# Kernel tuning notes

Measured on AMD Instinct MI355X. Metric: run time of the kernel, lower is better.

The kernel has to match this reference:

```python
import jax, jax.numpy as jnp
import numpy as np

N, E = 16384, 524288
IN_C, H1, H2 = 128, 128, 64
EDGE_F = 16
NB = 10                      # binary outputs
MC_GROUPS = (4, 6)           # multi-class group sizes (proto, service)
NC = 10                      # continuous outputs
EPS = 1e-5


def setup_inputs() -> dict:
    key = jax.random.key(0)
    ks = jax.random.split(key, 16)
    def lin(k, fan_in, fan_out):
        s = 1.0 / np.sqrt(fan_in)
        kw, kb = jax.random.split(k)
        return (jax.random.uniform(kw, (fan_in, fan_out), jnp.float32, -s, s),
                jax.random.uniform(kb, (fan_out,), jnp.float32, -s, s))
    w1, b1 = lin(ks[0], IN_C, H1)
    w2, b2 = lin(ks[1], H1, H2)
    w_bin, b_bin = lin(ks[2], H2, NB)
    w_mc, b_mc = lin(ks[3], H2, sum(MC_GROUPS))
    w_cont, b_cont = lin(ks[4], H2, NC)
    w_edge, b_edge = lin(ks[5], 2 * H2, EDGE_F)
    return {
        "x": jax.random.normal(ks[6], (N, IN_C), jnp.float32),
        "edge_index": jax.random.randint(ks[7], (2, E), 0, N, jnp.int64),
        "edge_attr": jax.random.normal(ks[8], (E, EDGE_F), jnp.float32),
        "w1": w1, "b1": b1,
        "bn1_g": jnp.ones((H1,), jnp.float32), "bn1_b": jnp.zeros((H1,), jnp.float32),
        "w2": w2, "b2": b2,
        "bn2_g": jnp.ones((H2,), jnp.float32), "bn2_b": jnp.zeros((H2,), jnp.float32),
        "w_bin": w_bin, "b_bin": b_bin,
        "w_mc": w_mc, "b_mc": b_mc,
        "w_cont": w_cont, "b_cont": b_cont,
        "w_edge": w_edge, "b_edge": b_edge,
    }


def _gcn(x, w, b, src, dst, norm, n):
    # GCNConv: x' = D^-1/2 (A+I) D^-1/2 (x W) + b
    h = x @ w
    msg = h[src] * norm[:, None]
    agg = jax.ops.segment_sum(msg, dst, num_segments=n)
    return agg + b


def _bn(h, g, b):
    m = jnp.mean(h, axis=0)
    v = jnp.var(h, axis=0)
    return g * (h - m) * jax.lax.rsqrt(v + EPS) + b


def reference(x, edge_index, edge_attr, w1, b1, bn1_g, bn1_b, w2, b2, bn2_g, bn2_b,
              w_bin, b_bin, w_mc, b_mc, w_cont, b_cont, w_edge, b_edge):
    n = x.shape[0]
    loops = jnp.arange(n, dtype=edge_index.dtype)
    src = jnp.concatenate([edge_index[0], loops])
    dst = jnp.concatenate([edge_index[1], loops])
    deg = jax.ops.segment_sum(jnp.ones_like(src, dtype=x.dtype), dst, num_segments=n)
    dis = jax.lax.rsqrt(deg)  # deg >= 1 thanks to self-loops
    norm = dis[src] * dis[dst]

    h = jax.nn.relu(_bn(_gcn(x, w1, b1, src, dst, norm, n), bn1_g, bn1_b))
    z = jax.nn.relu(_bn(_gcn(h, w2, b2, src, dst, norm, n), bn2_g, bn2_b))

    # node feature reconstruction: [binary sigmoid | per-group softmax | continuous]
    binary = jax.nn.sigmoid(z @ w_bin + b_bin)
    mc_logits = z @ w_mc + b_mc
    mc_parts, s = [], 0
    for g in MC_GROUPS:
        mc_parts.append(jax.nn.softmax(mc_logits[:, s:s + g], axis=1))
        s += g
    cont = z @ w_cont + b_cont
    reconstructed_x = jnp.concatenate([binary] + mc_parts + [cont], axis=1)

    adj = z @ z.T  # [N, N]

    edge_emb = jnp.concatenate([z[edge_index[0]], z[edge_index[1]]], axis=1)
    edge_features = edge_emb @ w_edge + b_edge
    return (reconstructed_x, adj, edge_features)
```

## Files before the change

kernel.cpp:

```cpp
#include <hip/hip_runtime.h>
#include <hip/hip_bf16.h>
#include <math.h>


constexpr int kN = 16384;
constexpr int kE = 524288;
constexpr float kEps = 1e-5f;

typedef __attribute__((ext_vector_type(8))) short short8v;
typedef __attribute__((ext_vector_type(4))) float f32x4;

__device__ inline float bf2f(unsigned short u) {
  return __uint_as_float(((unsigned)u) << 16);
}

__global__ void zero_kernel(int* counts, float* sums1, float* sums2,
                            const float* __restrict__ we, __hip_bfloat16* wfr) {
  int i = blockIdx.x * 256 + threadIdx.x;
  if (i < kN) counts[i] = 0;
  if (i < 256) sums1[i] = 0.f;
  if (i < 128) sums2[i] = 0.f;
  if (i < 2048) {
    int f = i >> 9, l = (i >> 3) & 63, j = i & 7;
    int lr = l & 15, lg = l >> 4;
    int krow = f * 32 + lg * 8 + j;
    wfr[i] = __float2bfloat16(we[krow * 16 + lr]);
  }
}

__global__ void hist_kernel(const int* __restrict__ dst, int* __restrict__ counts) {
  int e = blockIdx.x * 256 + threadIdx.x;
  if (e < kE) atomicAdd(&counts[dst[e]], 1);
}

__global__ __launch_bounds__(1024) void scan_kernel(const int* __restrict__ counts,
    int* __restrict__ offsets, int* __restrict__ pos, float* __restrict__ dis) {
  __shared__ int wave_tot[16];
  int tid = threadIdx.x;
  int base = tid * 16;
  int loc[16];
  int s = 0;
#pragma unroll
  for (int i = 0; i < 16; i++) { loc[i] = s; s += counts[base + i]; }
  int lane = tid & 63, wv = tid >> 6;
  int incl = s;
#pragma unroll
  for (int d = 1; d < 64; d <<= 1) {
    int v = __shfl_up(incl, d, 64);
    if (lane >= d) incl += v;
  }
  if (lane == 63) wave_tot[wv] = incl;
  __syncthreads();
  int woff = 0;
  for (int i = 0; i < wv; i++) woff += wave_tot[i];
  int excl = woff + incl - s;
#pragma unroll
  for (int i = 0; i < 16; i++) {
    int o = excl + loc[i];
    offsets[base + i] = o;
    pos[base + i] = o;
    dis[base + i] = rsqrtf((float)counts[base + i] + 1.0f);
  }
}

__global__ void fill_kernel(const int* __restrict__ src, const int* __restrict__ dst,
                            int* __restrict__ pos, int* __restrict__ csr_src) {
  int e = blockIdx.x * 256 + threadIdx.x;
  if (e < kE) {
    int d = dst[e];
    int p = atomicAdd(&pos[d], 1);
    csr_src[p] = src[e];
  }
}

__global__ __launch_bounds__(256) void gemm1_kernel(
    const float* __restrict__ A, const float* __restrict__ W,
    const float* __restrict__ dis, __hip_bfloat16* __restrict__ out) {
  constexpr int BC = 128, NJ = 8, WF4 = 4;
  __shared__ float xs[64 * 33];
  __shared__ float wsh[32 * BC];
  int tid = threadIdx.x;
  int tx = tid & 15, ty = tid >> 4;
  int r0 = blockIdx.x * 64;
  float acc[4][NJ];
#pragma unroll
  for (int r = 0; r < 4; r++)
#pragma unroll
    for (int j = 0; j < NJ; j++) acc[r][j] = 0.f;

  for (int kb = 0; kb < 128; kb += 32) {
    __syncthreads();
#pragma unroll
    for (int q = 0; q < 2; q++) {
      int f = tid + q * 256;
      int row = f >> 3, kq = f & 7;
      float4 v = *(const float4*)(A + (size_t)(r0 + row) * 128 + kb + kq * 4);
      int bb = row * 33 + kq * 4;
      xs[bb + 0] = v.x; xs[bb + 1] = v.y; xs[bb + 2] = v.z; xs[bb + 3] = v.w;
    }
#pragma unroll
    for (int q = 0; q < WF4; q++) {
      int f = tid + q * 256;
      int k = f / (BC / 4), cq = f % (BC / 4);
      *(float4*)&wsh[k * BC + cq * 4] =
          *(const float4*)(W + (size_t)(kb + k) * BC + cq * 4);
    }
    __syncthreads();
#pragma unroll
    for (int kk = 0; kk < 32; kk++) {
      float av[4];
#pragma unroll
      for (int r = 0; r < 4; r++) av[r] = xs[(ty * 4 + r) * 33 + kk];
#pragma unroll
      for (int j = 0; j < NJ; j++) {
        float bv = wsh[kk * BC + tx + j * 16];
#pragma unroll
        for (int r = 0; r < 4; r++) acc[r][j] = fmaf(av[r], bv, acc[r][j]);
      }
    }
  }
#pragma unroll
  for (int r = 0; r < 4; r++) {
    int row = r0 + ty * 4 + r;
    float dr = dis[row];
#pragma unroll
    for (int j = 0; j < NJ; j++)
      out[(size_t)row * BC + tx + j * 16] = __float2bfloat16(acc[r][j] * dr);
  }
}

__global__ __launch_bounds__(256) void gemm2_kernel(
    const unsigned short* __restrict__ A, const float* __restrict__ W,
    const float* __restrict__ sums, const float* __restrict__ g,
    const float* __restrict__ b, const float* __restrict__ dis,
    __hip_bfloat16* __restrict__ out) {
  constexpr int BC = 64, NJ = 4, WF4 = 2;
  __shared__ float xs[64 * 33];
  __shared__ float wsh[32 * BC];
  __shared__ float s_scl[128], s_shf[128];
  int tid = threadIdx.x;
  if (tid < 128) {
    float mean = sums[tid] / (float)kN;
    float var = sums[128 + tid] / (float)kN - mean * mean;
    float inv = rsqrtf(var + kEps);
    float sc = g[tid] * inv;
    s_scl[tid] = sc;
    s_shf[tid] = b[tid] - mean * sc;
  }
  int tx = tid & 15, ty = tid >> 4;
  int r0 = blockIdx.x * 64;
  float acc[4][NJ];
#pragma unroll
  for (int r = 0; r < 4; r++)
#pragma unroll
    for (int j = 0; j < NJ; j++) acc[r][j] = 0.f;

  for (int kb = 0; kb < 128; kb += 32) {
    __syncthreads();
    {
      int row = tid >> 2, kq = tid & 3;
      short8v v8 = *(const short8v*)(A + (size_t)(r0 + row) * 128 + kb + kq * 8);
      int bb = row * 33 + kq * 8;
#pragma unroll
      for (int j = 0; j < 8; j++) {
        int c = kb + kq * 8 + j;
        float v = bf2f((unsigned short)v8[j]);
        xs[bb + j] = fmaxf(0.f, fmaf(v, s_scl[c], s_shf[c]));
      }
    }
#pragma unroll
    for (int q = 0; q < WF4; q++) {
      int f = tid + q * 256;
      int k = f / (BC / 4), cq = f % (BC / 4);
      *(float4*)&wsh[k * BC + cq * 4] =
          *(const float4*)(W + (size_t)(kb + k) * BC + cq * 4);
    }
    __syncthreads();
#pragma unroll
    for (int kk = 0; kk < 32; kk++) {
      float av[4];
#pragma unroll
      for (int r = 0; r < 4; r++) av[r] = xs[(ty * 4 + r) * 33 + kk];
#pragma unroll
      for (int j = 0; j < NJ; j++) {
        float bv = wsh[kk * BC + tx + j * 16];
#pragma unroll
        for (int r = 0; r < 4; r++) acc[r][j] = fmaf(av[r], bv, acc[r][j]);
      }
    }
  }
#pragma unroll
  for (int r = 0; r < 4; r++) {
    int row = r0 + ty * 4 + r;
    float dr = dis[row];
#pragma unroll
    for (int j = 0; j < NJ; j++)
      out[(size_t)row * BC + tx + j * 16] = __float2bfloat16(acc[r][j] * dr);
  }
}

template <int C, bool OBF16>
__global__ void agg_kernel(const unsigned short* __restrict__ hs,
                           const int* __restrict__ csr_src, const int* __restrict__ offsets,
                           const int* __restrict__ counts, const float* __restrict__ dis,
                           void* __restrict__ tout) {
  int d = blockIdx.x;
  int c = threadIdx.x;
  float acc = bf2f(hs[(size_t)d * C + c]);
  int s0 = offsets[d];
  int n = counts[d];
  int i = 0;
  for (; i + 4 <= n; i += 4) {
    int sa = csr_src[s0 + i];
    int sb = csr_src[s0 + i + 1];
    int sc = csr_src[s0 + i + 2];
    int sd = csr_src[s0 + i + 3];
    float va = bf2f(hs[(size_t)sa * C + c]);
    float vb = bf2f(hs[(size_t)sb * C + c]);
    float vc = bf2f(hs[(size_t)sc * C + c]);
    float vd = bf2f(hs[(size_t)sd * C + c]);
    acc += va; acc += vb; acc += vc; acc += vd;
  }
  for (; i < n; i++) acc += bf2f(hs[(size_t)csr_src[s0 + i] * C + c]);
  float r = acc * dis[d];
  if constexpr (OBF16)
    ((__hip_bfloat16*)tout)[(size_t)d * C + c] = __float2bfloat16(r);
  else
    ((float*)tout)[(size_t)d * C + c] = r;
}

template <int C, bool BF16>
__global__ __launch_bounds__(256) void stats_kernel(const void* __restrict__ t,
                                                    float* __restrict__ sums) {
  constexpr int RP = 256 / C;
  int c = threadIdx.x % C;
  int rr = threadIdx.x / C;
  float s = 0.f, s2 = 0.f;
  for (int r = blockIdx.x * RP + rr; r < kN; r += gridDim.x * RP) {
    float v;
    if constexpr (BF16) v = bf2f(((const unsigned short*)t)[(size_t)r * C + c]);
    else v = ((const float*)t)[(size_t)r * C + c];
    s += v;
    s2 += v * v;
  }
  atomicAdd(&sums[c], s);
  atomicAdd(&sums[C + c], s2);
}

__global__ __launch_bounds__(256) void applyz_kernel(const float* __restrict__ t2,
    const float* __restrict__ sums, const float* __restrict__ g,
    const float* __restrict__ b, float* __restrict__ zf,
    __hip_bfloat16* __restrict__ zb) {
  __shared__ float s_scl[64], s_shf[64];
  int tid = threadIdx.x;
  if (tid < 64) {
    float mean = sums[tid] / (float)kN;
    float var = sums[64 + tid] / (float)kN - mean * mean;
    float inv = rsqrtf(var + kEps);
    float sc = g[tid] * inv;
    s_scl[tid] = sc;
    s_shf[tid] = b[tid] - mean * sc;
  }
  __syncthreads();
  int i = blockIdx.x * 256 + tid;
  int c = i & 63;
  float v = fmaxf(0.f, fmaf(t2[i], s_scl[c], s_shf[c]));
  zf[i] = v;
  zb[i] = __float2bfloat16(v);
}

__global__ __launch_bounds__(256) void heads_kernel(const float* __restrict__ zf,
    const float* __restrict__ wbin, const float* __restrict__ bbin,
    const float* __restrict__ wmc, const float* __restrict__ bmc,
    const float* __restrict__ wcont, const float* __restrict__ bcont,
    float* __restrict__ out0) {
  __shared__ float wT[30 * 64];
  __shared__ float bias[32];
  int tid = threadIdx.x;
  for (int idx = tid; idx < 1920; idx += 256) {
    int j = idx >> 6, k = idx & 63;
    const float* src = (j < 10) ? wbin : (j < 20) ? wmc : wcont;
    wT[idx] = src[k * 10 + (j % 10)];
  }
  if (tid < 30)
    bias[tid] = (tid < 10) ? bbin[tid] : (tid < 20) ? bmc[tid - 10] : bcont[tid - 20];
  __syncthreads();
  int n = blockIdx.x * 256 + tid;
  float zr[64];
  const float4* z4 = (const float4*)(zf + (size_t)n * 64);
#pragma unroll
  for (int q = 0; q < 16; q++) {
    float4 v = z4[q];
    zr[4 * q] = v.x; zr[4 * q + 1] = v.y; zr[4 * q + 2] = v.z; zr[4 * q + 3] = v.w;
  }
  float acc[30];
#pragma unroll
  for (int j = 0; j < 30; j++) {
    float s = bias[j];
#pragma unroll
    for (int kc = 0; kc < 16; kc++) {
      f32x4 wv = *(const f32x4*)&wT[j * 64 + kc * 4];
      s = fmaf(zr[4 * kc + 0], wv.x, s);
      s = fmaf(zr[4 * kc + 1], wv.y, s);
      s = fmaf(zr[4 * kc + 2], wv.z, s);
      s = fmaf(zr[4 * kc + 3], wv.w, s);
    }
    acc[j] = s;
  }
  float* o = out0 + (size_t)n * 30;
#pragma unroll
  for (int j = 0; j < 10; j++) o[j] = 1.f / (1.f + expf(-acc[j]));
  float m1 = fmaxf(fmaxf(acc[10], acc[11]), fmaxf(acc[12], acc[13]));
  float e1[4], s1 = 0.f;
#pragma unroll
  for (int j = 0; j < 4; j++) { e1[j] = expf(acc[10 + j] - m1); s1 += e1[j]; }
#pragma unroll
  for (int j = 0; j < 4; j++) o[10 + j] = e1[j] / s1;
  float m2 = acc[14];
#pragma unroll
  for (int j = 15; j < 20; j++) m2 = fmaxf(m2, acc[j]);
  float e2[6], s2 = 0.f;
#pragma unroll
  for (int j = 0; j < 6; j++) { e2[j] = expf(acc[14 + j] - m2); s2 += e2[j]; }
#pragma unroll
  for (int j = 0; j < 6; j++) o[14 + j] = e2[j] / s2;
#pragma unroll
  for (int j = 0; j < 10; j++) o[20 + j] = acc[20 + j];
}

__global__ __launch_bounds__(256) void adj_kernel(const short* __restrict__ zb,
                                                  float* __restrict__ adj) {
  __shared__ float cs[128 * 132];
  int tid = threadIdx.x;
  int wid = tid >> 6, lane = tid & 63;
  int li0 = (wid >> 1) * 64;
  int lj0 = (wid & 1) * 64;
  int i0 = blockIdx.x * 128 + li0;
  int j0 = blockIdx.y * 128 + lj0;
  int lr = lane & 15, lg = lane >> 4;
  short8v a[4][2], b[4][2];
#pragma unroll
  for (int mt = 0; mt < 4; mt++)
#pragma unroll
    for (int ks = 0; ks < 2; ks++)
      a[mt][ks] = *(const short8v*)(zb + (size_t)(i0 + mt * 16 + lr) * 64 + ks * 32 + lg * 8);
#pragma unroll
  for (int nt = 0; nt < 4; nt++)
#pragma unroll
    for (int ks = 0; ks < 2; ks++)
      b[nt][ks] = *(const short8v*)(zb + (size_t)(j0 + nt * 16 + lr) * 64 + ks * 32 + lg * 8);
  f32x4 acc[4][4];
#pragma unroll
  for (int mt = 0; mt < 4; mt++)
#pragma unroll
    for (int nt = 0; nt < 4; nt++) {
      f32x4 zz = {0.f, 0.f, 0.f, 0.f};
      acc[mt][nt] = zz;
    }
#pragma unroll
  for (int ks = 0; ks < 2; ks++)
#pragma unroll
    for (int mt = 0; mt < 4; mt++)
#pragma unroll
      for (int nt = 0; nt < 4; nt++)
        acc[mt][nt] = __builtin_amdgcn_mfma_f32_16x16x32_bf16(a[mt][ks], b[nt][ks],
                                                              acc[mt][nt], 0, 0, 0);
#pragma unroll
  for (int mt = 0; mt < 4; mt++)
#pragma unroll
    for (int nt = 0; nt < 4; nt++)
#pragma unroll
      for (int r = 0; r < 4; r++)
        cs[(li0 + mt * 16 + lg * 4 + r) * 132 + lj0 + nt * 16 + lr] = acc[mt][nt][r];
  __syncthreads();
  int row = tid >> 5;
  int c4 = tid & 31;
  size_t gbase = (size_t)(blockIdx.x * 128 + row) * kN + blockIdx.y * 128 + c4 * 4;
  const float* lbase = &cs[row * 132 + c4 * 4];
#pragma unroll
  for (int it = 0; it < 16; it++) {
    f32x4 v = *(const f32x4*)(lbase + it * 8 * 132);
    *(f32x4*)(adj + gbase + (size_t)it * 8 * kN) = v;
  }
}

__global__ __launch_bounds__(256) void edge_mfma_kernel(const short* __restrict__ zb,
    const int* __restrict__ srcs, const int* __restrict__ dsts,
    const short* __restrict__ wfr, const float* __restrict__ be,
    float* __restrict__ eout) {
  int tid = threadIdx.x;
  int wv = tid >> 6, lane = tid & 63;
  int gw = blockIdx.x * 4 + wv;
  int lr = lane & 15, lg = lane >> 4;
  short8v bfr[4];
#pragma unroll
  for (int f = 0; f < 4; f++)
    bfr[f] = *(const short8v*)(wfr + ((size_t)f * 64 + lane) * 8);
  float bias = be[lr];
  for (int t = 0; t < 8; t++) {
    int e0 = (gw * 8 + t) * 16;
    int se = srcs[e0 + lr], de = dsts[e0 + lr];
    short8v a0 = *(const short8v*)(zb + (size_t)se * 64 + lg * 8);
    short8v a1 = *(const short8v*)(zb + (size_t)se * 64 + 32 + lg * 8);
    short8v a2 = *(const short8v*)(zb + (size_t)de * 64 + lg * 8);
    short8v a3 = *(const short8v*)(zb + (size_t)de * 64 + 32 + lg * 8);
    f32x4 acc = {0.f, 0.f, 0.f, 0.f};
    acc = __builtin_amdgcn_mfma_f32_16x16x32_bf16(a0, bfr[0], acc, 0, 0, 0);
    acc = __builtin_amdgcn_mfma_f32_16x16x32_bf16(a1, bfr[1], acc, 0, 0, 0);
    acc = __builtin_amdgcn_mfma_f32_16x16x32_bf16(a2, bfr[2], acc, 0, 0, 0);
    acc = __builtin_amdgcn_mfma_f32_16x16x32_bf16(a3, bfr[3], acc, 0, 0, 0);
#pragma unroll
    for (int r = 0; r < 4; r++)
      eout[(size_t)(e0 + lg * 4 + r) * 16 + lr] = acc[r] + bias;
  }
}

extern "C" void kernel_launch(void* const* d_in, const int* in_sizes, int n_in,
                              void* d_out, int out_size, void* d_ws, size_t ws_size,
                              hipStream_t stream) {
  const float* x      = (const float*)d_in[0];
  const int*   ei     = (const int*)d_in[1];
  const float* w1     = (const float*)d_in[3];
  const float* bn1_g  = (const float*)d_in[5];
  const float* bn1_b  = (const float*)d_in[6];
  const float* w2     = (const float*)d_in[7];
  const float* bn2_g  = (const float*)d_in[9];
  const float* bn2_b  = (const float*)d_in[10];
  const float* w_bin  = (const float*)d_in[11];
  const float* b_bin  = (const float*)d_in[12];
  const float* w_mc   = (const float*)d_in[13];
  const float* b_mc   = (const float*)d_in[14];
  const float* w_cont = (const float*)d_in[15];
  const float* b_cont = (const float*)d_in[16];
  const float* w_edge = (const float*)d_in[17];
  const float* b_edge = (const float*)d_in[18];

  float* out0 = (float*)d_out;
  float* adj  = out0 + (size_t)kN * 30;
  float* eout = adj + (size_t)kN * kN;

  char* wp = (char*)d_ws;
  auto alloc = [&](size_t bytes) {
    char* p = wp;
    wp += (bytes + 255) & ~(size_t)255;
    return p;
  };
  int*   counts  = (int*)alloc((size_t)kN * 4);
  int*   offsets = (int*)alloc((size_t)kN * 4);
  int*   pos     = (int*)alloc((size_t)kN * 4);
  int*   csr_src = (int*)alloc((size_t)kE * 4);
  float* dis     = (float*)alloc((size_t)kN * 4);
  float* sums1   = (float*)alloc(256 * 4);
  float* sums2   = (float*)alloc(128 * 4);
  __hip_bfloat16* hs1 = (__hip_bfloat16*)alloc((size_t)kN * 128 * 2);
  __hip_bfloat16* t1  = (__hip_bfloat16*)alloc((size_t)kN * 128 * 2);
  __hip_bfloat16* hs2 = (__hip_bfloat16*)alloc((size_t)kN * 64 * 2);
  float* t2      = (float*)alloc((size_t)kN * 64 * 4);
  float* zf      = (float*)alloc((size_t)kN * 64 * 4);
  __hip_bfloat16* zb  = (__hip_bfloat16*)alloc((size_t)kN * 64 * 2);
  __hip_bfloat16* wfr = (__hip_bfloat16*)alloc(2048 * 2);

  const int* esrc = ei;
  const int* edst = ei + kE;

  zero_kernel<<<dim3(64), dim3(256), 0, stream>>>(counts, sums1, sums2, w_edge, wfr);
  hist_kernel<<<dim3(2048), dim3(256), 0, stream>>>(edst, counts);
  scan_kernel<<<dim3(1), dim3(1024), 0, stream>>>(counts, offsets, pos, dis);
  fill_kernel<<<dim3(2048), dim3(256), 0, stream>>>(esrc, edst, pos, csr_src);

  gemm1_kernel<<<dim3(kN / 64), dim3(256), 0, stream>>>(x, w1, dis, hs1);
  agg_kernel<128, true><<<dim3(kN), dim3(128), 0, stream>>>(
      (const unsigned short*)hs1, csr_src, offsets, counts, dis, t1);
  stats_kernel<128, true><<<dim3(256), dim3(256), 0, stream>>>(t1, sums1);

  gemm2_kernel<<<dim3(kN / 64), dim3(256), 0, stream>>>(
      (const unsigned short*)t1, w2, sums1, bn1_g, bn1_b, dis, hs2);
  agg_kernel<64, false><<<dim3(kN), dim3(64), 0, stream>>>(
      (const unsigned short*)hs2, csr_src, offsets, counts, dis, t2);
  stats_kernel<64, false><<<dim3(256), dim3(256), 0, stream>>>(t2, sums2);

  applyz_kernel<<<dim3(kN * 64 / 256), dim3(256), 0, stream>>>(
      t2, sums2, bn2_g, bn2_b, zf, zb);

  heads_kernel<<<dim3(kN / 256), dim3(256), 0, stream>>>(
      zf, w_bin, b_bin, w_mc, b_mc, w_cont, b_cont, out0);
  adj_kernel<<<dim3(kN / 128, kN / 128), dim3(256), 0, stream>>>((const short*)zb, adj);
  edge_mfma_kernel<<<dim3(1024), dim3(256), 0, stream>>>(
      (const short*)zb, esrc, edst, (const short*)wfr, b_edge, eout);
}
```

Measured before the change: 442.2 us.

## Vectorize neighbor aggregation per wave, fuse BN2 into heads, stage edge stores

Both aggregation kernels move from one thread per channel to one wavefront per node. Lane groups load 16-byte vectors of neighbor rows over interleaved edges and are combined with cross-lane shuffles. The BN2 apply/ReLU is folded into the heads kernel, which also writes the bf16 z, so the fp32 z buffer and one launch go away. Edge-feature outputs are staged through shared memory so each lane writes a contiguous float4, at the cost of extra LDS traffic and less parallelism per node for low-degree nodes.

```diff
diff --git a/kernel.cpp b/kernel.cpp
--- a/kernel.cpp
+++ b/kernel.cpp
@@ -12,6 +12,10 @@
 
 __device__ inline float bf2f(unsigned short u) {
   return __uint_as_float(((unsigned)u) << 16);
+}
+__device__ inline unsigned short f2bf(float f) {
+  unsigned u = __float_as_uint(f);
+  return (unsigned short)((u + 0x7fff + ((u >> 16) & 1)) >> 16);
 }
 
 __global__ void zero_kernel(int* counts, float* sums1, float* sums2,
@@ -199,34 +203,104 @@
   }
 }
 
-template <int C, bool OBF16>
-__global__ void agg_kernel(const unsigned short* __restrict__ hs,
-                           const int* __restrict__ csr_src, const int* __restrict__ offsets,
-                           const int* __restrict__ counts, const float* __restrict__ dis,
-                           void* __restrict__ tout) {
-  int d = blockIdx.x;
-  int c = threadIdx.x;
-  float acc = bf2f(hs[(size_t)d * C + c]);
-  int s0 = offsets[d];
-  int n = counts[d];
-  int i = 0;
-  for (; i + 4 <= n; i += 4) {
+__global__ __launch_bounds__(256) void agg1_kernel(const unsigned short* __restrict__ hs,
+    const int* __restrict__ csr_src, const int* __restrict__ offsets,
+    const int* __restrict__ counts, const float* __restrict__ dis,
+    unsigned short* __restrict__ t1) {
+  int tid = threadIdx.x;
+  int wv = tid >> 6, lane = tid & 63;
+  int d = blockIdx.x * 4 + wv;
+  int g = lane >> 4, l = lane & 15;
+  float acc[8];
+  if (g == 0) {
+    short8v v = *(const short8v*)(hs + (size_t)d * 128 + l * 8);
+#pragma unroll
+    for (int j = 0; j < 8; j++) acc[j] = bf2f((unsigned short)v[j]);
+  } else {
+#pragma unroll
+    for (int j = 0; j < 8; j++) acc[j] = 0.f;
+  }
+  int s0 = offsets[d], n = counts[d];
+  int i = g;
+  for (; i + 4 < n; i += 8) {
     int sa = csr_src[s0 + i];
-    int sb = csr_src[s0 + i + 1];
-    int sc = csr_src[s0 + i + 2];
-    int sd = csr_src[s0 + i + 3];
-    float va = bf2f(hs[(size_t)sa * C + c]);
-    float vb = bf2f(hs[(size_t)sb * C + c]);
-    float vc = bf2f(hs[(size_t)sc * C + c]);
-    float vd = bf2f(hs[(size_t)sd * C + c]);
-    acc += va; acc += vb; acc += vc; acc += vd;
-  }
-  for (; i < n; i++) acc += bf2f(hs[(size_t)csr_src[s0 + i] * C + c]);
-  float r = acc * dis[d];
-  if constexpr (OBF16)
-    ((__hip_bfloat16*)tout)[(size_t)d * C + c] = __float2bfloat16(r);
-  else
-    ((float*)tout)[(size_t)d * C + c] = r;
+    int sb = csr_src[s0 + i + 4];
+    short8v va = *(const short8v*)(hs + (size_t)sa * 128 + l * 8);
+    short8v vb = *(const short8v*)(hs + (size_t)sb * 128 + l * 8);
+#pragma unroll
+    for (int j = 0; j < 8; j++) acc[j] += bf2f((unsigned short)va[j]);
+#pragma unroll
+    for (int j = 0; j < 8; j++) acc[j] += bf2f((unsigned short)vb[j]);
+  }
+  if (i < n) {
+    int sa = csr_src[s0 + i];
+    short8v va = *(const short8v*)(hs + (size_t)sa * 128 + l * 8);
+#pragma unroll
+    for (int j = 0; j < 8; j++) acc[j] += bf2f((unsigned short)va[j]);
+  }
+#pragma unroll
+  for (int j = 0; j < 8; j++) {
+    acc[j] += __shfl_xor(acc[j], 16, 64);
+    acc[j] += __shfl_xor(acc[j], 32, 64);
+  }
+  if (g == 0) {
+    float dd = dis[d];
+    short8v o;
+#pragma unroll
+    for (int j = 0; j < 8; j++) o[j] = (short)f2bf(acc[j] * dd);
+    *(short8v*)(t1 + (size_t)d * 128 + l * 8) = o;
+  }
+}
+
+__global__ __launch_bounds__(256) void agg2_kernel(const unsigned short* __restrict__ hs,
+    const int* __restrict__ csr_src, const int* __restrict__ offsets,
+    const int* __restrict__ counts, const float* __restrict__ dis,
+    float* __restrict__ t2) {
+  int tid = threadIdx.x;
+  int wv = tid >> 6, lane = tid & 63;
+  int d = blockIdx.x * 4 + wv;
+  int g = lane >> 3, l = lane & 7;
+  float acc[8];
+  if (g == 0) {
+    short8v v = *(const short8v*)(hs + (size_t)d * 64 + l * 8);
+#pragma unroll
+    for (int j = 0; j < 8; j++) acc[j] = bf2f((unsigned short)v[j]);
+  } else {
+#pragma unroll
+    for (int j = 0; j < 8; j++) acc[j] = 0.f;
+  }
+  int s0 = offsets[d], n = counts[d];
+  int i = g;
+  for (; i + 8 < n; i += 16) {
+    int sa = csr_src[s0 + i];
+    int sb = csr_src[s0 + i + 8];
+    short8v va = *(const short8v*)(hs + (size_t)sa * 64 + l * 8);
+    short8v vb = *(const short8v*)(hs + (size_t)sb * 64 + l * 8);
+#pragma unroll
+    for (int j = 0; j < 8; j++) acc[j] += bf2f((unsigned short)va[j]);
+#pragma unroll
+    for (int j = 0; j < 8; j++) acc[j] += bf2f((unsigned short)vb[j]);
+  }
+  if (i < n) {
+    int sa = csr_src[s0 + i];
+    short8v va = *(const short8v*)(hs + (size_t)sa * 64 + l * 8);
+#pragma unroll
+    for (int j = 0; j < 8; j++) acc[j] += bf2f((unsigned short)va[j]);
+  }
+#pragma unroll
+  for (int j = 0; j < 8; j++) {
+    acc[j] += __shfl_xor(acc[j], 8, 64);
+    acc[j] += __shfl_xor(acc[j], 16, 64);
+    acc[j] += __shfl_xor(acc[j], 32, 64);
+  }
+  if (g == 0) {
+    float dd = dis[d];
+    float* o = t2 + (size_t)d * 64 + l * 8;
+    f32x4 o0 = {acc[0] * dd, acc[1] * dd, acc[2] * dd, acc[3] * dd};
+    f32x4 o1 = {acc[4] * dd, acc[5] * dd, acc[6] * dd, acc[7] * dd};
+    *(f32x4*)o = o0;
+    *(f32x4*)(o + 4) = o1;
+  }
 }
 
 template <int C, bool BF16>
@@ -247,51 +321,51 @@
   atomicAdd(&sums[C + c], s2);
 }
 
-__global__ __launch_bounds__(256) void applyz_kernel(const float* __restrict__ t2,
-    const float* __restrict__ sums, const float* __restrict__ g,
-    const float* __restrict__ b, float* __restrict__ zf,
-    __hip_bfloat16* __restrict__ zb) {
+__global__ __launch_bounds__(256) void zheads_kernel(const float* __restrict__ t2,
+    const float* __restrict__ sums, const float* __restrict__ gg,
+    const float* __restrict__ bb2,
+    const float* __restrict__ wbin, const float* __restrict__ bbin,
+    const float* __restrict__ wmc, const float* __restrict__ bmc,
+    const float* __restrict__ wcont, const float* __restrict__ bcont,
+    float* __restrict__ out0, unsigned short* __restrict__ zb) {
+  __shared__ float wT[30 * 64];
+  __shared__ float bias[32];
   __shared__ float s_scl[64], s_shf[64];
   int tid = threadIdx.x;
+  for (int idx = tid; idx < 1920; idx += 256) {
+    int j = idx >> 6, k = idx & 63;
+    const float* src = (j < 10) ? wbin : (j < 20) ? wmc : wcont;
+    wT[idx] = src[k * 10 + (j % 10)];
+  }
+  if (tid < 30)
+    bias[tid] = (tid < 10) ? bbin[tid] : (tid < 20) ? bmc[tid - 10] : bcont[tid - 20];
   if (tid < 64) {
     float mean = sums[tid] / (float)kN;
     float var = sums[64 + tid] / (float)kN - mean * mean;
     float inv = rsqrtf(var + kEps);
-    float sc = g[tid] * inv;
+    float sc = gg[tid] * inv;
     s_scl[tid] = sc;
-    s_shf[tid] = b[tid] - mean * sc;
-  }
-  __syncthreads();
-  int i = blockIdx.x * 256 + tid;
-  int c = i & 63;
-  float v = fmaxf(0.f, fmaf(t2[i], s_scl[c], s_shf[c]));
-  zf[i] = v;
-  zb[i] = __float2bfloat16(v);
-}
-
-__global__ __launch_bounds__(256) void heads_kernel(const float* __restrict__ zf,
-    const float* __restrict__ wbin, const float* __restrict__ bbin,
-    const float* __restrict__ wmc, const float* __restrict__ bmc,
-    const float* __restrict__ wcont, const float* __restrict__ bcont,
-    float* __restrict__ out0) {
-  __shared__ float wT[30 * 64];
-  __shared__ float bias[32];
-  int tid = threadIdx.x;
-  for (int idx = tid; idx < 1920; idx += 256) {
-    int j = idx >> 6, k = idx & 63;
-    const float* src = (j < 10) ? wbin : (j < 20) ? wmc : wcont;
-    wT[idx] = src[k * 10 + (j % 10)];
-  }
-  if (tid < 30)
-    bias[tid] = (tid < 10) ? bbin[tid] : (tid < 20) ? bmc[tid - 10] : bcont[tid - 20];
+    s_shf[tid] = bb2[tid] - mean * sc;
+  }
   __syncthreads();
   int n = blockIdx.x * 256 + tid;
   float zr[64];
-  const float4* z4 = (const float4*)(zf + (size_t)n * 64);
+  const float4* t4 = (const float4*)(t2 + (size_t)n * 64);
 #pragma unroll
   for (int q = 0; q < 16; q++) {
-    float4 v = z4[q];
-    zr[4 * q] = v.x; zr[4 * q + 1] = v.y; zr[4 * q + 2] = v.z; zr[4 * q + 3] = v.w;
+    float4 v = t4[q];
+    zr[4 * q + 0] = fmaxf(0.f, fmaf(v.x, s_scl[4 * q + 0], s_shf[4 * q + 0]));
+    zr[4 * q + 1] = fmaxf(0.f, fmaf(v.y, s_scl[4 * q + 1], s_shf[4 * q + 1]));
+    zr[4 * q + 2] = fmaxf(0.f, fmaf(v.z, s_scl[4 * q + 2], s_shf[4 * q + 2]));
+    zr[4 * q + 3] = fmaxf(0.f, fmaf(v.w, s_scl[4 * q + 3], s_shf[4 * q + 3]));
+  }
+  unsigned short* zrow = zb + (size_t)n * 64;
+#pragma unroll
+  for (int q = 0; q < 8; q++) {
+    short8v o;
+#pragma unroll
+    for (int j = 0; j < 8; j++) o[j] = (short)f2bf(zr[q * 8 + j]);
+    *(short8v*)(zrow + q * 8) = o;
   }
   float acc[30];
 #pragma unroll
@@ -388,6 +462,7 @@
     const int* __restrict__ srcs, const int* __restrict__ dsts,
     const short* __restrict__ wfr, const float* __restrict__ be,
     float* __restrict__ eout) {
+  __shared__ float es[4][256];
   int tid = threadIdx.x;
   int wv = tid >> 6, lane = tid & 63;
   int gw = blockIdx.x * 4 + wv;
@@ -411,7 +486,9 @@
     acc = __builtin_amdgcn_mfma_f32_16x16x32_bf16(a3, bfr[3], acc, 0, 0, 0);
 #pragma unroll
     for (int r = 0; r < 4; r++)
-      eout[(size_t)(e0 + lg * 4 + r) * 16 + lr] = acc[r] + bias;
+      es[wv][(lg * 4 + r) * 16 + lr] = acc[r] + bias;
+    f32x4 v = *(const f32x4*)&es[wv][lane * 4];
+    *(f32x4*)(eout + (size_t)e0 * 16 + lane * 4) = v;
   }
 }
 
@@ -452,12 +529,11 @@
   float* dis     = (float*)alloc((size_t)kN * 4);
   float* sums1   = (float*)alloc(256 * 4);
   float* sums2   = (float*)alloc(128 * 4);
-  __hip_bfloat16* hs1 = (__hip_bfloat16*)alloc((size_t)kN * 128 * 2);
-  __hip_bfloat16* t1  = (__hip_bfloat16*)alloc((size_t)kN * 128 * 2);
-  __hip_bfloat16* hs2 = (__hip_bfloat16*)alloc((size_t)kN * 64 * 2);
+  unsigned short* hs1 = (unsigned short*)alloc((size_t)kN * 128 * 2);
+  unsigned short* t1  = (unsigned short*)alloc((size_t)kN * 128 * 2);
+  unsigned short* hs2 = (unsigned short*)alloc((size_t)kN * 64 * 2);
   float* t2      = (float*)alloc((size_t)kN * 64 * 4);
-  float* zf      = (float*)alloc((size_t)kN * 64 * 4);
-  __hip_bfloat16* zb  = (__hip_bfloat16*)alloc((size_t)kN * 64 * 2);
+  unsigned short* zb  = (unsigned short*)alloc((size_t)kN * 64 * 2);
   __hip_bfloat16* wfr = (__hip_bfloat16*)alloc(2048 * 2);
 
   const int* esrc = ei;
@@ -468,22 +544,21 @@
   scan_kernel<<<dim3(1), dim3(1024), 0, stream>>>(counts, offsets, pos, dis);
   fill_kernel<<<dim3(2048), dim3(256), 0, stream>>>(esrc, edst, pos, csr_src);
 
-  gemm1_kernel<<<dim3(kN / 64), dim3(256), 0, stream>>>(x, w1, dis, hs1);
-  agg_kernel<128, true><<<dim3(kN), dim3(128), 0, stream>>>(
-      (const unsigned short*)hs1, csr_src, offsets, counts, dis, t1);
+  gemm1_kernel<<<dim3(kN / 64), dim3(256), 0, stream>>>(
+      x, w1, dis, (__hip_bfloat16*)hs1);
+  agg1_kernel<<<dim3(kN / 4), dim3(256), 0, stream>>>(
+      hs1, csr_src, offsets, counts, dis, t1);
   stats_kernel<128, true><<<dim3(256), dim3(256), 0, stream>>>(t1, sums1);
 
   gemm2_kernel<<<dim3(kN / 64), dim3(256), 0, stream>>>(
-      (const unsigned short*)t1, w2, sums1, bn1_g, bn1_b, dis, hs2);
-  agg_kernel<64, false><<<dim3(kN), dim3(64), 0, stream>>>(
-      (const unsigned short*)hs2, csr_src, offsets, counts, dis, t2);
+      t1, w2, sums1, bn1_g, bn1_b, dis, (__hip_bfloat16*)hs2);
+  agg2_kernel<<<dim3(kN / 4), dim3(256), 0, stream>>>(
+      hs2, csr_src, offsets, counts, dis, t2);
   stats_kernel<64, false><<<dim3(256), dim3(256), 0, stream>>>(t2, sums2);
 
-  applyz_kernel<<<dim3(kN * 64 / 256), dim3(256), 0, stream>>>(
-      t2, sums2, bn2_g, bn2_b, zf, zb);
-
-  heads_kernel<<<dim3(kN / 256), dim3(256), 0, stream>>>(
-      zf, w_bin, b_bin, w_mc, b_mc, w_cont, b_cont, out0);
+  zheads_kernel<<<dim3(kN / 256), dim3(256), 0, stream>>>(
+      t2, sums2, bn2_g, bn2_b, w_bin, b_bin, w_mc, b_mc, w_cont, b_cont, out0, zb);
+
   adj_kernel<<<dim3(kN / 128, kN / 128), dim3(256), 0, stream>>>((const short*)zb, adj);
   edge_mfma_kernel<<<dim3(1024), dim3(256), 0, stream>>>(
       (const short*)zb, esrc, edst, (const short*)wfr, b_edge, eout);
```

Result: faster. 430.1 us (-2.7%).
